# Optimization experiments

Measured on AMD Instinct MI355X. Metric: run time of the kernel, lower is better.

Reference implementation:

```python
import jax, jax.numpy as jnp
import numpy as np

D = 1024
K_LOW1 = D // 4  # first low-precision segment of the contraction dim
K_LOW2 = D // 4  # last low-precision segment


def mix_precision_matmul(x, w):
    """x: [B,N,d], w: [d,3d]. Contraction dim d is split into
    low1 | high | low2 column bands; low bands run in fp16, high in fp32.
    Partial products are summed to give the full matmul result."""
    d = x.shape[-1]
    w1 = w[:K_LOW1]
    wh = w[K_LOW1:d - K_LOW2]
    w2 = w[d - K_LOW2:]
    y1 = jnp.matmul(x[..., :K_LOW1].astype(jnp.float16), w1.astype(jnp.float16)).astype(jnp.float32)
    yh = jnp.matmul(x[..., K_LOW1:d - K_LOW2], wh)
    y2 = jnp.matmul(x[..., d - K_LOW2:].astype(jnp.float16), w2.astype(jnp.float16)).astype(jnp.float32)
    return y1 + yh + y2


def setup_inputs() -> dict:
    key = jax.random.key(0)
    k1, k2, k3, k4 = jax.random.split(key, 4)
    B, N, d = 8, 2048, D
    x = jax.random.normal(k1, (B, N, d), dtype=jnp.float32)
    weight_qkv = jax.random.normal(k2, (d, 3 * d), dtype=jnp.float32) * (d ** -0.5)
    out_w = jax.random.normal(k3, (d, d), dtype=jnp.float32) * (d ** -0.5)
    out_b = jax.random.normal(k4, (d,), dtype=jnp.float32) * 0.01
    return {"x": x, "weight_qkv": weight_qkv, "out_w": out_w, "out_b": out_b}


def reference(x, weight_qkv, out_w, out_b):
    d = x.shape[-1]
    qkv = mix_precision_matmul(x, weight_qkv)  # [B, N, 3d]
    q, k, v = jnp.split(qkv, 3, axis=-1)
    q = q / jnp.sqrt(jnp.asarray(d, dtype=q.dtype))
    qk = jnp.einsum('bqd,bkd->bqk', q, k)      # [B, N, N]
    s = jax.nn.softmax(qk, axis=-1)
    y = jnp.einsum('bqk,bkd->bqd', s, v)       # [B, N, d]
    return jnp.matmul(y, out_w.T) + out_b
```

## Files before the change

kernel.cpp:

```cpp
#include <hip/hip_runtime.h>

typedef __attribute__((ext_vector_type(8))) _Float16 half8;
typedef __attribute__((ext_vector_type(4))) _Float16 half4;
typedef __attribute__((ext_vector_type(4))) float floatx4;

#define DEVI __device__ __forceinline__

DEVI void gload_lds16(const _Float16* g, _Float16* l) {
    __builtin_amdgcn_global_load_lds(
        (const __attribute__((address_space(1))) void*)g,
        (__attribute__((address_space(3))) void*)l, 16, 0, 0);
}

#define WAITV(N) asm volatile("s_waitcnt vmcnt(" #N ")" ::: "memory")
#define BAR() __builtin_amdgcn_s_barrier()


template <int K>
DEVI void stage_u(const _Float16* __restrict__ A, const _Float16* __restrict__ B,
                  _Float16* lds, int t, int u, int tid) {
    constexpr int NT = K >> 6;
    const int tt = t < NT ? t : NT - 1;
    const _Float16* sp = ((u < 2) ? A : B) + (size_t)((u & 1) * 128) * K + (size_t)tt * 64;
    _Float16* dst = lds + ((t & 1) * 4 + u) * 8192;
    const int s0 = tid, s1 = tid + 512;
    const int r0 = s0 >> 3, c0 = (s0 & 7) ^ (r0 & 7);
    const int r1 = s1 >> 3, c1 = (s1 & 7) ^ (r1 & 7);
    gload_lds16(sp + (size_t)r0 * K + c0 * 8, dst + s0 * 8);
    gload_lds16(sp + (size_t)r1 * K + c1 * 8, dst + s1 * 8);
}

template <int K>
DEVI void gemmdp(const _Float16* __restrict__ A, const _Float16* __restrict__ B,
                 _Float16* lds, floatx4 acc[8][4], int tid)
{
    const int lane = tid & 63, w = tid >> 6;
    const int wm = w >> 2, wn = w & 3;
    const int lr = lane & 15, quad = lane >> 4, xr = lr & 7;
    const int co0 = (quad ^ xr) << 3;
    const int co1 = ((4 + quad) ^ xr) << 3;
    const int brow = (wn & 1) * 64;
    const int aU = wm, bU = 2 + (wn >> 1);
    constexpr int NT = K >> 6;

    stage_u<K>(A, B, lds, 0, 0, tid); stage_u<K>(A, B, lds, 0, 1, tid);
    stage_u<K>(A, B, lds, 0, 2, tid); stage_u<K>(A, B, lds, 0, 3, tid);

    for (int T = 0; T < NT; ++T) {
        stage_u<K>(A, B, lds, T + 1, 0, tid); stage_u<K>(A, B, lds, T + 1, 1, tid);
        stage_u<K>(A, B, lds, T + 1, 2, tid); stage_u<K>(A, B, lds, T + 1, 3, tid);
        WAITV(8);
        BAR();

        const _Float16* ua = lds + ((T & 1) * 4 + aU) * 8192;
        const _Float16* ub = lds + ((T & 1) * 4 + bU) * 8192;
        half8 bf[4][2];
#pragma unroll
        for (int ni = 0; ni < 4; ++ni) {
            bf[ni][0] = *(const half8*)&ub[(brow + ni * 16 + lr) * 64 + co0];
            bf[ni][1] = *(const half8*)&ub[(brow + ni * 16 + lr) * 64 + co1];
        }
        half8 af[8][2];
#pragma unroll
        for (int mi = 0; mi < 8; ++mi) {
            af[mi][0] = *(const half8*)&ua[(mi * 16 + lr) * 64 + co0];
            af[mi][1] = *(const half8*)&ua[(mi * 16 + lr) * 64 + co1];
        }
        __builtin_amdgcn_s_setprio(1);
#pragma unroll
        for (int mi = 0; mi < 8; ++mi)
#pragma unroll
            for (int kk = 0; kk < 2; ++kk)
#pragma unroll
                for (int ni = 0; ni < 4; ++ni)
                    acc[mi][ni] = __builtin_amdgcn_mfma_f32_16x16x32_f16(
                        af[mi][kk], bf[ni][kk], acc[mi][ni], 0, 0, 0);
        __builtin_amdgcn_s_setprio(0);
        BAR();
    }
    WAITV(0);
}

DEVI void zacc(floatx4 acc[8][4]) {
    const floatx4 zf = {0.f, 0.f, 0.f, 0.f};
#pragma unroll
    for (int mi = 0; mi < 8; ++mi)
#pragma unroll
        for (int ni = 0; ni < 4; ++ni) acc[mi][ni] = zf;
}

__global__ __launch_bounds__(256) void k_cast_x(const float* __restrict__ x, _Float16* __restrict__ xh) {
    size_t i = ((size_t)blockIdx.x * 256 + threadIdx.x) * 8;
    float4 v0 = *(const float4*)(x + i);
    float4 v1 = *(const float4*)(x + i + 4);
    float vv[8] = {v0.x, v0.y, v0.z, v0.w, v1.x, v1.y, v1.z, v1.w};
    half8 h;
#pragma unroll
    for (int j = 0; j < 8; ++j) h[j] = (_Float16)vv[j];
    *(half8*)(xh + i) = h;
}

__global__ __launch_bounds__(256) void k_prep_w(const float* __restrict__ w, _Float16* __restrict__ wh) {
    __shared__ float tile[32][33];
    const int n0 = blockIdx.x * 32, k0 = blockIdx.y * 32;
    const int t = threadIdx.x;
#pragma unroll
    for (int it = 0; it < 4; ++it) {
        int idx = it * 256 + t;
        int kk = idx >> 5, nn = idx & 31;
        tile[kk][nn] = w[(size_t)(k0 + kk) * 3072 + n0 + nn];
    }
    __syncthreads();
#pragma unroll
    for (int it = 0; it < 4; ++it) {
        int idx = it * 256 + t;
        int nn = idx >> 5, kk = idx & 31;
        wh[(size_t)(n0 + nn) * 1024 + k0 + kk] = (_Float16)tile[kk][nn];
    }
}

__global__ __launch_bounds__(256) void k_prep_ow(const float* __restrict__ ow, _Float16* __restrict__ owh) {
    size_t i = ((size_t)blockIdx.x * 256 + threadIdx.x) * 8;
    float4 v0 = *(const float4*)(ow + i);
    float4 v1 = *(const float4*)(ow + i + 4);
    float vv[8] = {v0.x, v0.y, v0.z, v0.w, v1.x, v1.y, v1.z, v1.w};
    half8 h;
#pragma unroll
    for (int j = 0; j < 8; ++j) h[j] = (_Float16)vv[j];
    *(half8*)(owh + i) = h;
}

__global__ __launch_bounds__(512, 2) void k_qkv256(
    const _Float16* __restrict__ xh, const _Float16* __restrict__ wh,
    _Float16* __restrict__ qh, _Float16* __restrict__ kh, _Float16* __restrict__ vT)
{
    __shared__ __align__(16) _Float16 L[65536];
    const int lin = blockIdx.x + 64 * blockIdx.y;
    const int xcd = lin & 7, j = lin >> 3;
    const int m0 = (xcd * 8 + (j & 7)) * 256, n0 = (j >> 3) * 256;
    const int tid = threadIdx.x;
    floatx4 acc[8][4];
    zacc(acc);
    gemmdp<1024>(xh + (size_t)m0 * 1024, wh + (size_t)n0 * 1024, L, acc, tid);

    const int lane = tid & 63, w = tid >> 6;
    const int lr = lane & 15, quad = lane >> 4;
    const int mb0 = m0 + (w >> 2) * 128 + quad * 4;
    const int nb0 = n0 + (w & 3) * 64 + lr;
    if (n0 < 1024) {
#pragma unroll
        for (int mi = 0; mi < 8; ++mi)
#pragma unroll
            for (int ni = 0; ni < 4; ++ni)
#pragma unroll
                for (int r = 0; r < 4; ++r)
                    qh[(size_t)(mb0 + mi * 16 + r) * 1024 + (nb0 + ni * 16)] =
                        (_Float16)(acc[mi][ni][r] * 0.03125f);
    } else if (n0 < 2048) {
#pragma unroll
        for (int mi = 0; mi < 8; ++mi)
#pragma unroll
            for (int ni = 0; ni < 4; ++ni)
#pragma unroll
                for (int r = 0; r < 4; ++r)
                    kh[(size_t)(mb0 + mi * 16 + r) * 1024 + (nb0 - 1024 + ni * 16)] =
                        (_Float16)acc[mi][ni][r];
    } else {
#pragma unroll
        for (int mi = 0; mi < 8; ++mi)
#pragma unroll
            for (int ni = 0; ni < 4; ++ni) {
                int mb = mb0 + mi * 16;
                int b = mb >> 11, ml = mb & 2047;
                int e = nb0 - 2048 + ni * 16;
                half4 pk;
#pragma unroll
                for (int r = 0; r < 4; ++r) pk[r] = (_Float16)acc[mi][ni][r];
                *(half4*)&vT[((size_t)b * 1024 + e) * 2048 + ml] = pk;
            }
    }
}

template <int EPI, int K, int MODE>
__global__ __launch_bounds__(512, 2) void k_g256(
    const _Float16* __restrict__ Ab, const _Float16* __restrict__ Bb,
    _Float16* __restrict__ C16, float* __restrict__ C32, const float* __restrict__ bias,
    unsigned long long sAz, unsigned long long sBz, unsigned long long sCz, int ldc)
{
    __shared__ __align__(16) _Float16 L[65536];
    const int gx = gridDim.x, gy = gridDim.y;
    const int lin = blockIdx.x + gx * (blockIdx.y + gy * blockIdx.z);
    const int xcd = lin & 7, j = lin >> 3;
    int bx, by, bz;
    if (MODE == 0) { bz = xcd; bx = j % gx; by = j / gx; }
    else           { bz = 0;   bx = xcd * (gx >> 3) + j % (gx >> 3); by = j / (gx >> 3); }
    const int m0 = bx * 256, n0 = by * 256;
    const int tid = threadIdx.x;
    floatx4 acc[8][4];
    zacc(acc);
    gemmdp<K>(Ab + (size_t)bz * sAz + (size_t)m0 * K,
              Bb + (size_t)bz * sBz + (size_t)n0 * K, L, acc, tid);

    const int lane = tid & 63, w = tid >> 6;
    const int lr = lane & 15, quad = lane >> 4;
    const int mb0 = m0 + (w >> 2) * 128 + quad * 4;
    const int nb0 = n0 + (w & 3) * 64 + lr;
#pragma unroll
    for (int mi = 0; mi < 8; ++mi)
#pragma unroll
        for (int ni = 0; ni < 4; ++ni)
#pragma unroll
            for (int r = 0; r < 4; ++r) {
                int m = mb0 + mi * 16 + r;
                int n = nb0 + ni * 16;
                if (EPI == 0)
                    C16[(size_t)bz * sCz + (size_t)m * ldc + n] = (_Float16)acc[mi][ni][r];
                else
                    C32[(size_t)m * ldc + n] = acc[mi][ni][r] + bias[n];
            }
}

DEVI float wred_max(float v) {
#pragma unroll
    for (int o = 32; o; o >>= 1) v = fmaxf(v, __shfl_xor(v, o, 64));
    return v;
}
DEVI float wred_sum(float v) {
#pragma unroll
    for (int o = 32; o; o >>= 1) v += __shfl_xor(v, o, 64);
    return v;
}

__global__ __launch_bounds__(256) void k_softmax(_Float16* __restrict__ S) {
    const size_t row = blockIdx.x;
    _Float16* p = S + row * 2048;
    const int t = threadIdx.x;
    __shared__ float redm[4], reds[4];
    float v[8];
    float mx = -3.4e38f;
#pragma unroll
    for (int i = 0; i < 8; ++i) { v[i] = (float)p[t + i * 256]; mx = fmaxf(mx, v[i]); }
    mx = wred_max(mx);
    if ((t & 63) == 0) redm[t >> 6] = mx;
    __syncthreads();
    mx = fmaxf(fmaxf(redm[0], redm[1]), fmaxf(redm[2], redm[3]));
    float s = 0.f;
#pragma unroll
    for (int i = 0; i < 8; ++i) { v[i] = __expf(v[i] - mx); s += v[i]; }
    s = wred_sum(s);
    if ((t & 63) == 0) reds[t >> 6] = s;
    __syncthreads();
    s = reds[0] + reds[1] + reds[2] + reds[3];
    float inv = 1.0f / s;
#pragma unroll
    for (int i = 0; i < 8; ++i) p[t + i * 256] = (_Float16)(v[i] * inv);
}

extern "C" void kernel_launch(void* const* d_in, const int* in_sizes, int n_in,
                              void* d_out, int out_size, void* d_ws, size_t ws_size,
                              hipStream_t stream) {
    const float* x  = (const float*)d_in[0];
    const float* wq = (const float*)d_in[1];
    const float* ow = (const float*)d_in[2];
    const float* ob = (const float*)d_in[3];
    float* out = (float*)d_out;

    char* ws = (char*)d_ws;
    _Float16* xh  = (_Float16*)(ws + 0);
    _Float16* wh  = (_Float16*)(ws + 33554432);
    _Float16* S   = (_Float16*)(ws + 0);
    _Float16* qh  = (_Float16*)(ws + 67108864);
    _Float16* kh  = (_Float16*)(ws + 100663296);
    _Float16* vT  = (_Float16*)(ws + 134217728);
    _Float16* owh = (_Float16*)(ws + 167772160);
    _Float16* y   = qh;

    if (ws_size < 180355072ull) return;

    hipLaunchKernelGGL(k_cast_x, dim3(8192), dim3(256), 0, stream, x, xh);
    hipLaunchKernelGGL(k_prep_w, dim3(96, 32), dim3(256), 0, stream, wq, wh);
    hipLaunchKernelGGL(k_qkv256, dim3(64, 12), dim3(512), 0, stream, xh, wh, qh, kh, vT);
    hipLaunchKernelGGL((k_g256<0, 1024, 0>), dim3(8, 8, 8), dim3(512), 0, stream,
                       qh, kh, S, (float*)nullptr, (const float*)nullptr,
                       2048ull * 1024, 2048ull * 1024, 2048ull * 2048, 2048);
    hipLaunchKernelGGL(k_prep_ow, dim3(512), dim3(256), 0, stream, ow, owh);
    hipLaunchKernelGGL(k_softmax, dim3(16384), dim3(256), 0, stream, S);
    hipLaunchKernelGGL((k_g256<0, 2048, 0>), dim3(8, 4, 8), dim3(512), 0, stream,
                       S, vT, y, (float*)nullptr, (const float*)nullptr,
                       2048ull * 2048, 1024ull * 2048, 2048ull * 1024, 1024);
    hipLaunchKernelGGL((k_g256<1, 1024, 1>), dim3(64, 4, 1), dim3(512), 0, stream,
                       y, owh, (_Float16*)nullptr, out, ob,
                       0ull, 0ull, 0ull, 1024);
}
```

Measured before the change: 425.3 us.

## Restructure GEMM main loop into 8-phase interleaved LDS-read/MFMA/global-load pipeline

Replaces the double-buffered GEMM loop with a four-quarter schedule per K-tile. Each quarter reads a small slice of A fragments, issues one unit of global-to-LDS staging, and runs a subset of MFMAs. B units are prefetched two tiles ahead while A units are prefetched one ahead. The aim is to overlap memory traffic and LDS reads with matrix-core work, and to cut register pressure by holding only 2 A fragments at a time. The cost is many more barriers per tile and tighter waitcnt reasoning, which risks stalls or races if the buffer reuse timing is wrong.

```diff
diff --git a/kernel.cpp b/kernel.cpp
--- a/kernel.cpp
+++ b/kernel.cpp
@@ -12,8 +12,10 @@
         (__attribute__((address_space(3))) void*)l, 16, 0, 0);
 }
 
-#define WAITV(N) asm volatile("s_waitcnt vmcnt(" #N ")" ::: "memory")
-#define BAR() __builtin_amdgcn_s_barrier()
+#define WAITV(N)  asm volatile("s_waitcnt vmcnt(" #N ")" ::: "memory")
+#define LGKM(N)   asm volatile("s_waitcnt lgkmcnt(" #N ")" ::: "memory")
+#define CFENCE()  asm volatile("" ::: "memory")
+#define BAR()     __builtin_amdgcn_s_barrier()
 
 
 template <int K>
@@ -30,8 +32,26 @@
     gload_lds16(sp + (size_t)r1 * K + c1 * 8, dst + s1 * 8);
 }
 
+#define RD_AF(q) \
+    af[0][0] = *(const half8*)&ua[((q) * 32 +  0 + lr) * 64 + co0]; \
+    af[0][1] = *(const half8*)&ua[((q) * 32 +  0 + lr) * 64 + co1]; \
+    af[1][0] = *(const half8*)&ua[((q) * 32 + 16 + lr) * 64 + co0]; \
+    af[1][1] = *(const half8*)&ua[((q) * 32 + 16 + lr) * 64 + co1];
+
+#define MFMA_Q(q) \
+    __builtin_amdgcn_s_setprio(1); \
+    _Pragma("unroll") \
+    for (int kk = 0; kk < 2; ++kk) \
+        _Pragma("unroll") \
+        for (int m2 = 0; m2 < 2; ++m2) \
+            _Pragma("unroll") \
+            for (int ni = 0; ni < 4; ++ni) \
+                acc[2 * (q) + m2][ni] = __builtin_amdgcn_mfma_f32_16x16x32_f16( \
+                    af[m2][kk], bf[ni][kk], acc[2 * (q) + m2][ni], 0, 0, 0); \
+    __builtin_amdgcn_s_setprio(0);
+
 template <int K>
-DEVI void gemmdp(const _Float16* __restrict__ A, const _Float16* __restrict__ B,
+DEVI void gemm8p(const _Float16* __restrict__ A, const _Float16* __restrict__ B,
                  _Float16* lds, floatx4 acc[8][4], int tid)
 {
     const int lane = tid & 63, w = tid >> 6;
@@ -45,37 +65,40 @@
 
     stage_u<K>(A, B, lds, 0, 0, tid); stage_u<K>(A, B, lds, 0, 1, tid);
     stage_u<K>(A, B, lds, 0, 2, tid); stage_u<K>(A, B, lds, 0, 3, tid);
+    stage_u<K>(A, B, lds, 1, 2, tid); stage_u<K>(A, B, lds, 1, 3, tid);
+    WAITV(4);
+    BAR();
 
     for (int T = 0; T < NT; ++T) {
-        stage_u<K>(A, B, lds, T + 1, 0, tid); stage_u<K>(A, B, lds, T + 1, 1, tid);
-        stage_u<K>(A, B, lds, T + 1, 2, tid); stage_u<K>(A, B, lds, T + 1, 3, tid);
-        WAITV(8);
-        BAR();
-
         const _Float16* ua = lds + ((T & 1) * 4 + aU) * 8192;
         const _Float16* ub = lds + ((T & 1) * 4 + bU) * 8192;
-        half8 bf[4][2];
+        half8 bf[4][2], af[2][2];
 #pragma unroll
         for (int ni = 0; ni < 4; ++ni) {
             bf[ni][0] = *(const half8*)&ub[(brow + ni * 16 + lr) * 64 + co0];
             bf[ni][1] = *(const half8*)&ub[(brow + ni * 16 + lr) * 64 + co1];
         }
-        half8 af[8][2];
-#pragma unroll
-        for (int mi = 0; mi < 8; ++mi) {
-            af[mi][0] = *(const half8*)&ua[(mi * 16 + lr) * 64 + co0];
-            af[mi][1] = *(const half8*)&ua[(mi * 16 + lr) * 64 + co1];
-        }
-        __builtin_amdgcn_s_setprio(1);
-#pragma unroll
-        for (int mi = 0; mi < 8; ++mi)
-#pragma unroll
-            for (int kk = 0; kk < 2; ++kk)
-#pragma unroll
-                for (int ni = 0; ni < 4; ++ni)
-                    acc[mi][ni] = __builtin_amdgcn_mfma_f32_16x16x32_f16(
-                        af[mi][kk], bf[ni][kk], acc[mi][ni], 0, 0, 0);
-        __builtin_amdgcn_s_setprio(0);
+        RD_AF(0);
+        stage_u<K>(A, B, lds, T + 1, 0, tid);
+        LGKM(8);
+        CFENCE(); BAR(); LGKM(0);
+        MFMA_Q(0);
+        BAR();
+        RD_AF(1);
+        stage_u<K>(A, B, lds, T + 1, 1, tid);
+        CFENCE(); BAR(); LGKM(0);
+        MFMA_Q(1);
+        BAR();
+        RD_AF(2);
+        stage_u<K>(A, B, lds, T + 2, 2, tid);
+        CFENCE(); BAR(); LGKM(0);
+        MFMA_Q(2);
+        BAR();
+        RD_AF(3);
+        stage_u<K>(A, B, lds, T + 2, 3, tid);
+        WAITV(4);
+        CFENCE(); BAR(); LGKM(0);
+        MFMA_Q(3);
         BAR();
     }
     WAITV(0);
@@ -141,7 +164,7 @@
     const int tid = threadIdx.x;
     floatx4 acc[8][4];
     zacc(acc);
-    gemmdp<1024>(xh + (size_t)m0 * 1024, wh + (size_t)n0 * 1024, L, acc, tid);
+    gemm8p<1024>(xh + (size_t)m0 * 1024, wh + (size_t)n0 * 1024, L, acc, tid);
 
     const int lane = tid & 63, w = tid >> 6;
     const int lr = lane & 15, quad = lane >> 4;
@@ -198,7 +221,7 @@
     const int tid = threadIdx.x;
     floatx4 acc[8][4];
     zacc(acc);
-    gemmdp<K>(Ab + (size_t)bz * sAz + (size_t)m0 * K,
+    gemm8p<K>(Ab + (size_t)bz * sAz + (size_t)m0 * K,
               Bb + (size_t)bz * sBz + (size_t)n0 * K, L, acc, tid);
 
     const int lane = tid & 63, w = tid >> 6;
```

After: 445.5 us. 1.05x slower.
